# Kernel optimization log

Hardware: AMD Instinct MI355X
Metric: run time of the kernel (lower is better)

## Reference

```python
import jax, jax.numpy as jnp
import numpy as np

D_MODEL = 1024
N_LAYERS = 4
EXPAND = 2
D_CONV = 4
D_STATE = 16
INTER = EXPAND * D_MODEL          # 2048
DT_RANK = (D_MODEL + 15) // 16    # 64, HF: math.ceil(d_model/16)
B_SZ = 4
SEQ = 1024
EPS = 1e-5


def setup_inputs() -> dict:
    key = jax.random.key(0)
    ks = jax.random.split(key, 8)
    nrm = lambda k, s: (0.02 * jax.random.normal(k, s)).astype(jnp.float32)
    return {
        "x": jax.random.normal(ks[0], (B_SZ, SEQ, D_MODEL), dtype=jnp.float32),
        "in_w": nrm(ks[1], (N_LAYERS, 2 * INTER, D_MODEL)),           # in_proj (no bias)
        "conv_w": nrm(ks[2], (N_LAYERS, INTER, D_CONV)),              # depthwise conv weight
        "conv_b": jnp.zeros((N_LAYERS, INTER), jnp.float32),           # conv bias
        "x_w": nrm(ks[3], (N_LAYERS, DT_RANK + 2 * D_STATE, INTER)),  # x_proj (no bias)
        "dt_w": nrm(ks[4], (N_LAYERS, INTER, DT_RANK)),               # dt_proj weight
        "dt_b": jax.random.uniform(ks[5], (N_LAYERS, INTER), minval=-4.0, maxval=-2.0).astype(jnp.float32),
        "A_log": jnp.tile(jnp.log(jnp.arange(1, D_STATE + 1, dtype=jnp.float32)), (N_LAYERS, INTER, 1)),
        "D": jnp.ones((N_LAYERS, INTER), jnp.float32),
        "out_w": nrm(ks[6], (N_LAYERS, D_MODEL, INTER)),              # out_proj (no bias)
        "norm_w": jnp.ones((N_LAYERS, D_MODEL), jnp.float32),          # per-block RMSNorm
        "norm_f_w": jnp.ones((D_MODEL,), jnp.float32),                 # final RMSNorm
    }


def _rmsnorm(x, w):
    return x * jax.lax.rsqrt(jnp.mean(x * x, axis=-1, keepdims=True) + EPS) * w


def _mixer(x, in_w, conv_w, conv_b, x_w, dt_w, dt_b, A_log, Dp, out_w):
    # x: [B, L, d_model]
    Bb = x.shape[0]
    proj = x @ in_w.T                              # [B, L, 2I]
    hs, gate = jnp.split(proj, 2, axis=-1)          # each [B, L, I]
    # causal depthwise conv over time
    hc = hs.transpose(0, 2, 1)                      # [B, I, L]
    hc = jnp.pad(hc, ((0, 0), (0, 0), (D_CONV - 1, 0)))
    hc = jax.lax.conv_general_dilated(
        hc, conv_w[:, None, :], (1,), 'VALID',
        dimension_numbers=('NCH', 'OIH', 'NCH'), feature_group_count=INTER)
    hc = hc + conv_b[None, :, None]
    u = jax.nn.silu(hc).transpose(0, 2, 1)          # [B, L, I]
    ssm = u @ x_w.T                                 # [B, L, dt_rank + 2N]
    dt, Bm, Cm = jnp.split(ssm, [DT_RANK, DT_RANK + D_STATE], axis=-1)
    dt = jax.nn.softplus(dt @ dt_w.T + dt_b)        # [B, L, I]
    A = -jnp.exp(A_log)                             # [I, N]

    def step(state, xs):
        dt_t, B_t, C_t, u_t = xs                    # [B,I], [B,N], [B,N], [B,I]
        dA = jnp.exp(dt_t[:, :, None] * A[None])    # [B, I, N]
        state = dA * state + (dt_t * u_t)[:, :, None] * B_t[:, None, :]
        y = jnp.einsum('bin,bn->bi', state, C_t)
        return state, y

    init = jnp.zeros((Bb, INTER, D_STATE), x.dtype)
    xs = (dt.transpose(1, 0, 2), Bm.transpose(1, 0, 2),
          Cm.transpose(1, 0, 2), u.transpose(1, 0, 2))
    _, ys = jax.lax.scan(step, init, xs)            # ys: [L, B, I]
    y = ys.transpose(1, 0, 2) + u * Dp              # skip term D * u
    y = y * jax.nn.silu(gate)
    return y @ out_w.T                              # [B, L, d_model]


def reference(x, in_w, conv_w, conv_b, x_w, dt_w, dt_b, A_log, D, out_w, norm_w, norm_f_w):
    h = x
    for l in range(N_LAYERS):
        h = h + _mixer(_rmsnorm(h, norm_w[l]), in_w[l], conv_w[l], conv_b[l],
                       x_w[l], dt_w[l], dt_b[l], A_log[l], D[l], out_w[l])
    return _rmsnorm(h, norm_f_w)
```

## Files before the change

kernel.cpp:

```cpp
#include <hip/hip_runtime.h>
#include <hip/hip_bf16.h>
#include <math.h>

#define D_MODEL 1024
#define N_LAYERS 4
#define INTER 2048
#define D_CONV 4
#define D_STATE 16
#define DT_RANK 64
#define B_SZ 4
#define SEQ 1024
#define TOK (B_SZ*SEQ)
#define XROWS 128
#define EPSV 1e-5f
#define GCH 64
#define TC (SEQ/GCH)
#define KSPL 8
#define OSPL 2

typedef unsigned short u16;
typedef unsigned int u32;
typedef __attribute__((ext_vector_type(8))) short bf16x8;
typedef __attribute__((ext_vector_type(4))) short s16x4;
typedef __attribute__((ext_vector_type(4))) float f32x4;

__device__ __forceinline__ u16 f2b(float f) {
    union { float f; unsigned u; } v; v.f = f;
    unsigned r = v.u + 0x7fffu + ((v.u >> 16) & 1u);
    return (u16)(r >> 16);
}
__device__ __forceinline__ float b2f(u16 h) {
    union { unsigned u; float f; } v; v.u = ((unsigned)h) << 16;
    return v.f;
}
__device__ __forceinline__ float silu(float x) {
    return x / (1.f + __expf(-x));
}
__device__ __forceinline__ void gload16(const void* g, void* l) {
    __builtin_amdgcn_global_load_lds(
        (const __attribute__((address_space(1))) void*)g,
        (__attribute__((address_space(3))) void*)l, 16, 0, 0);
}

__global__ __launch_bounds__(512, 2)
void gemm256_k(const u16* __restrict__ A, const u16* __restrict__ B,
               u16* __restrict__ C, int K, int ldc)
{
    __shared__ u16 lds[2][2][256 * 64];
    const int tid  = threadIdx.x;
    const int lane = tid & 63;
    const int wid  = tid >> 6;
    const int wr   = wid >> 2;
    const int wc   = wid & 3;
    const int hwid = blockIdx.y * gridDim.x + blockIdx.x;
    const int work = (hwid & 7) * 32 + (hwid >> 3);
    const int row0 = (work >> 4) * 256;
    const int col0 = (work & 15) * 256;
    const int r16   = lane & 15;
    const int khalf = lane >> 4;

    auto ld1 = [&](int buf, int k0, int l) {
        int op = l >> 2;
        int c  = tid + (l & 3) * 512;
        int r  = c >> 3;
        int ds = c & 7;
        int sc = (ds ^ (r & 7)) * 8;
        const u16* src = op ? &B[(size_t)(col0 + r) * K + k0 + sc]
                            : &A[(size_t)(row0 + r) * K + k0 + sc];
        gload16(src, &lds[buf][op][c * 8]);
    };
    auto stage2 = [&](int buf, int k0, int pair) {
        if (pair == 0)      { ld1(buf, k0, 0); ld1(buf, k0, 2); }
        else if (pair == 1) { ld1(buf, k0, 4); ld1(buf, k0, 5); }
        else if (pair == 2) { ld1(buf, k0, 6); ld1(buf, k0, 7); }
        else                { ld1(buf, k0, 1); ld1(buf, k0, 3); }
    };
    auto rdA = [&](int buf, int mrow, int ks) -> bf16x8 {
        int row  = wr * 128 + mrow + r16;
        int phys = ((ks << 2) | khalf) ^ (row & 7);
        return *(const bf16x8*)&lds[buf][0][row * 64 + phys * 8];
    };
    auto rdB = [&](int buf, int nrow, int ks) -> bf16x8 {
        int row  = wc * 64 + nrow + r16;
        int phys = ((ks << 2) | khalf) ^ (row & 7);
        return *(const bf16x8*)&lds[buf][1][row * 64 + phys * 8];
    };

    f32x4 acc[8][4];
#pragma unroll
    for (int m = 0; m < 8; ++m)
#pragma unroll
        for (int n = 0; n < 4; ++n)
            acc[m][n] = (f32x4)0.f;

    bf16x8 af[4][2], bf2[2][2];

#define PHASE_MFMA(MH, NH) do {                                               \
    asm volatile("s_waitcnt lgkmcnt(0)" ::: "memory");                        \
    __builtin_amdgcn_sched_barrier(0);                                        \
    __builtin_amdgcn_s_setprio(1);                                            \
    _Pragma("unroll")                                                         \
    for (int ks = 0; ks < 2; ++ks)                                            \
        _Pragma("unroll")                                                     \
        for (int m = 0; m < 4; ++m)                                           \
            _Pragma("unroll")                                                 \
            for (int n = 0; n < 2; ++n)                                       \
                acc[(MH)*4+m][(NH)*2+n] =                                     \
                    __builtin_amdgcn_mfma_f32_16x16x32_bf16(                  \
                        af[m][ks], bf2[n][ks], acc[(MH)*4+m][(NH)*2+n],0,0,0);\
    __builtin_amdgcn_s_setprio(0);                                            \
} while (0)

    const int nt = K >> 6;
    stage2(0, 0, 0); stage2(0, 0, 1); stage2(0, 0, 2); stage2(0, 0, 3);
    asm volatile("s_waitcnt vmcnt(2)" ::: "memory");
    __builtin_amdgcn_s_barrier();

    for (int j = 0; j < nt; ++j) {
        const int buf = j & 1;
        const int nb  = buf ^ 1;
        const int k1  = (j + 1) << 6;
        const bool pf = (j + 1 < nt);
        if (pf) stage2(nb, k1, 0);
#pragma unroll
        for (int m = 0; m < 4; ++m) {
            af[m][0] = rdA(buf, m * 16, 0); af[m][1] = rdA(buf, m * 16, 1);
        }
#pragma unroll
        for (int n = 0; n < 2; ++n) {
            bf2[n][0] = rdB(buf, n * 16, 0); bf2[n][1] = rdB(buf, n * 16, 1);
        }
        __builtin_amdgcn_s_barrier();
        PHASE_MFMA(0, 0);
        __builtin_amdgcn_s_barrier();
        if (pf) stage2(nb, k1, 1);
#pragma unroll
        for (int n = 0; n < 2; ++n) {
            bf2[n][0] = rdB(buf, 32 + n * 16, 0); bf2[n][1] = rdB(buf, 32 + n * 16, 1);
        }
        __builtin_amdgcn_s_barrier();
        PHASE_MFMA(0, 1);
        if (pf) { asm volatile("s_waitcnt vmcnt(4)" ::: "memory"); }
        else    { asm volatile("s_waitcnt vmcnt(0)" ::: "memory"); }
        __builtin_amdgcn_s_barrier();
        if (pf) stage2(nb, k1, 2);
#pragma unroll
        for (int m = 0; m < 4; ++m) {
            af[m][0] = rdA(buf, 64 + m * 16, 0); af[m][1] = rdA(buf, 64 + m * 16, 1);
        }
        __builtin_amdgcn_s_barrier();
        PHASE_MFMA(1, 1);
        __builtin_amdgcn_s_barrier();
        if (pf) stage2(nb, k1, 3);
#pragma unroll
        for (int n = 0; n < 2; ++n) {
            bf2[n][0] = rdB(buf, n * 16, 0); bf2[n][1] = rdB(buf, n * 16, 1);
        }
        __builtin_amdgcn_s_barrier();
        PHASE_MFMA(1, 0);
        asm volatile("s_waitcnt vmcnt(2)" ::: "memory");
        __builtin_amdgcn_s_barrier();
    }
#undef PHASE_MFMA

    const int orow = row0 + wr * 128;
    const int ocol = col0 + wc * 64;
#pragma unroll
    for (int am = 0; am < 8; ++am)
#pragma unroll
        for (int an = 0; an < 4; ++an)
#pragma unroll
            for (int r = 0; r < 4; ++r) {
                int rr = orow + am * 16 + khalf * 4 + r;
                int cc = ocol + an * 16 + r16;
                C[(size_t)rr * ldc + cc] = f2b(acc[am][an][r]);
            }
}

template<int EPI, int NPX = 1>
__global__ __launch_bounds__(256)
void gemm_bt(const u16* __restrict__ A, const u16* __restrict__ B,
             void* __restrict__ C, const float* __restrict__ aux,
             int K, int lda, int ldc, size_t pstride)
{
    __shared__ u16 As[3][128 * 32];
    __shared__ u16 Bs[3][128 * 32];
    const int tid  = threadIdx.x;
    const int lane = tid & 63;
    const int w    = tid >> 6;
    const int wr   = w >> 1, wc = w & 1;
    const int row0 = blockIdx.y * 128;
    int col0 = blockIdx.x * 128;
    if (EPI == 4) {
        int part = blockIdx.x / NPX;
        col0 = (blockIdx.x % NPX) * 128;
        A += (size_t)part * K;
        B += (size_t)part * K;
        C = (void*)((float*)C + (size_t)part * pstride);
    }
    const int r16   = lane & 15;
    const int khalf = lane >> 4;
    const int kslot = khalf ^ ((r16 >> 1) & 3);

    auto stage = [&](int buf, int k0) {
#pragma unroll
        for (int c = 0; c < 2; ++c) {
            int chunk = tid + c * 256;
            int r  = chunk >> 2;
            int j  = chunk & 3;
            int k8 = (j ^ ((r >> 1) & 3)) * 8;
            gload16(&A[(size_t)(row0 + r) * lda + k0 + k8], &As[buf][chunk * 8]);
            gload16(&B[(size_t)(col0 + r) * lda + k0 + k8], &Bs[buf][chunk * 8]);
        }
    };

    f32x4 acc[4][4];
#pragma unroll
    for (int m = 0; m < 4; ++m)
#pragma unroll
        for (int n = 0; n < 4; ++n)
            acc[m][n] = (f32x4)0.f;

    const int nt = K >> 5;
    stage(0, 0);
    if (nt > 1) stage(1, 32);

    int cur = 0, sb = 2;
    for (int t = 0; t < nt; ++t) {
        if (t + 2 < nt) {
            stage(sb, (t + 2) << 5);
            asm volatile("s_waitcnt vmcnt(8)" ::: "memory");
        } else if (t + 1 < nt) {
            asm volatile("s_waitcnt vmcnt(4)" ::: "memory");
        } else {
            asm volatile("s_waitcnt vmcnt(0)" ::: "memory");
        }
        __builtin_amdgcn_s_barrier();

        bf16x8 af[4], bfr[4];
#pragma unroll
        for (int m = 0; m < 4; ++m)
            af[m]  = *(const bf16x8*)&As[cur][(wr * 64 + m * 16 + r16) * 32 + kslot * 8];
#pragma unroll
        for (int n = 0; n < 4; ++n)
            bfr[n] = *(const bf16x8*)&Bs[cur][(wc * 64 + n * 16 + r16) * 32 + kslot * 8];
#pragma unroll
        for (int m = 0; m < 4; ++m)
#pragma unroll
            for (int n = 0; n < 4; ++n)
                acc[m][n] = __builtin_amdgcn_mfma_f32_16x16x32_bf16(
                    af[m], bfr[n], acc[m][n], 0, 0, 0);

        __builtin_amdgcn_sched_barrier(0);
        asm volatile("s_waitcnt lgkmcnt(0)" ::: "memory");
        __builtin_amdgcn_s_barrier();
        cur = (cur == 2) ? 0 : cur + 1;
        sb  = (sb  == 2) ? 0 : sb  + 1;
    }

    const int orow = row0 + wr * 64;
    const int ocol = col0 + wc * 64;
#pragma unroll
    for (int m = 0; m < 4; ++m)
#pragma unroll
        for (int n = 0; n < 4; ++n) {
#pragma unroll
            for (int r = 0; r < 4; ++r) {
                int rr = orow + m * 16 + khalf * 4 + r;
                int cc = ocol + n * 16 + r16;
                float v = acc[m][n][r];
                size_t o = (size_t)rr * ldc + cc;
                if (EPI == 0 || EPI == 4) {
                    ((float*)C)[o] = v;
                } else if (EPI == 2) {
                    float x = v + aux[cc];
                    float sp = (x > 20.f) ? x : log1pf(__expf(x));
                    ((u16*)C)[o] = f2b(sp);
                }
            }
        }
}

__global__ __launch_bounds__(256)
void xred_k(const float* __restrict__ part, float* __restrict__ ssm,
            u16* __restrict__ dtr)
{
    int idx = blockIdx.x * 256 + threadIdx.x;
    int row = idx >> 5;
    int col = (idx & 31) * 4;
    size_t o = (size_t)row * XROWS + col;
    const size_t stride = (size_t)TOK * XROWS;
    f32x4 v = *(const f32x4*)&part[o];
#pragma unroll
    for (int p = 1; p < KSPL; ++p)
        v += *(const f32x4*)&part[o + p * stride];
    *(f32x4*)&ssm[o] = v;
    if (col < DT_RANK) {
        s16x4 d;
#pragma unroll
        for (int j = 0; j < 4; ++j) d[j] = (short)f2b(v[j]);
        *(s16x4*)&dtr[(size_t)row * DT_RANK + col] = d;
    }
}

template<int OUTBF>
__global__ __launch_bounds__(256)
void rmsnorm_k(const float* __restrict__ in, const float* __restrict__ w,
               void* __restrict__ out)
{
    __shared__ float red[4];
    const int row = blockIdx.x;
    const int tid = threadIdx.x;
    const float* r = in + (size_t)row * D_MODEL;
    f32x4 v = *(const f32x4*)&r[tid * 4];
    float ss = v[0]*v[0] + v[1]*v[1] + v[2]*v[2] + v[3]*v[3];
#pragma unroll
    for (int m = 32; m >= 1; m >>= 1) ss += __shfl_xor(ss, m, 64);
    if ((tid & 63) == 0) red[tid >> 6] = ss;
    __syncthreads();
    if (tid == 0) {
        float s = red[0] + red[1] + red[2] + red[3];
        red[0] = rsqrtf(s / (float)D_MODEL + EPSV);
    }
    __syncthreads();
    float sc = red[0];
    if (OUTBF) {
        u16* o = (u16*)out + (size_t)row * D_MODEL + tid * 4;
#pragma unroll
        for (int j = 0; j < 4; ++j) o[j] = f2b(v[j] * sc * w[tid * 4 + j]);
    } else {
        float* o = (float*)out + (size_t)row * D_MODEL + tid * 4;
#pragma unroll
        for (int j = 0; j < 4; ++j) o[j] = v[j] * sc * w[tid * 4 + j];
    }
}

template<int OUTBF, int WRITEH>
__global__ __launch_bounds__(256)
void rmsnorm_res_k(const float* __restrict__ hin, const float* __restrict__ p,
                   const float* __restrict__ w, float* __restrict__ hout,
                   void* __restrict__ out)
{
    __shared__ float red[4];
    const int row = blockIdx.x;
    const int tid = threadIdx.x;
    const size_t o4 = (size_t)row * D_MODEL + tid * 4;
    f32x4 v  = *(const f32x4*)&hin[o4];
    f32x4 p0 = *(const f32x4*)&p[o4];
    f32x4 p1 = *(const f32x4*)&p[(size_t)TOK * D_MODEL + o4];
    v += p0 + p1;
    if (WRITEH) *(f32x4*)&hout[o4] = v;
    float ss = v[0]*v[0] + v[1]*v[1] + v[2]*v[2] + v[3]*v[3];
#pragma unroll
    for (int m = 32; m >= 1; m >>= 1) ss += __shfl_xor(ss, m, 64);
    if ((tid & 63) == 0) red[tid >> 6] = ss;
    __syncthreads();
    if (tid == 0) {
        float s = red[0] + red[1] + red[2] + red[3];
        red[0] = rsqrtf(s / (float)D_MODEL + EPSV);
    }
    __syncthreads();
    float sc = red[0];
    if (OUTBF) {
        u16* o = (u16*)out + o4;
#pragma unroll
        for (int j = 0; j < 4; ++j) o[j] = f2b(v[j] * sc * w[tid * 4 + j]);
    } else {
        float* o = (float*)out + o4;
#pragma unroll
        for (int j = 0; j < 4; ++j) o[j] = v[j] * sc * w[tid * 4 + j];
    }
}

__global__ __launch_bounds__(256)
void conv_silu_k(const u16* __restrict__ projbf, const float* __restrict__ w,
                 const float* __restrict__ bias, u16* __restrict__ ubf)
{
    const int row = blockIdx.x;
    const int t   = row & (SEQ - 1);
    const int i0  = threadIdx.x * 8;
    float acc[8];
    {
        f32x4 b0 = *(const f32x4*)&bias[i0];
        f32x4 b1 = *(const f32x4*)&bias[i0 + 4];
#pragma unroll
        for (int j = 0; j < 4; ++j) { acc[j] = b0[j]; acc[j + 4] = b1[j]; }
    }
    f32x4 wv[8];
#pragma unroll
    for (int j = 0; j < 8; ++j)
        wv[j] = *(const f32x4*)&w[(i0 + j) * 4];
#pragma unroll
    for (int k = 0; k < 4; ++k) {
        int tt = t - 3 + k;
        if (tt >= 0) {
            bf16x8 hv = *(const bf16x8*)&projbf[(size_t)(row - 3 + k) * 4096 + i0];
#pragma unroll
            for (int j = 0; j < 8; ++j)
                acc[j] += b2f((u16)hv[j]) * wv[j][k];
        }
    }
    bf16x8 o;
#pragma unroll
    for (int j = 0; j < 8; ++j)
        o[j] = (short)f2b(silu(acc[j]));
    *(bf16x8*)&ubf[(size_t)row * INTER + i0] = o;
}

__global__ __launch_bounds__(256)
void achk_k(const float* __restrict__ Alog, int* __restrict__ flags)
{
    int idx = blockIdx.x * 256 + threadIdx.x;
    if (idx >= N_LAYERS * INTER * D_STATE) return;
    int l = idx / (INTER * D_STATE);
    int n = idx & (D_STATE - 1);
    float ref = logf((float)(n + 1));
    if (fabsf(Alog[idx] - ref) > 1e-4f) atomicAnd(&flags[l], 0);
}

#define POWCH(W, p) \
    float p##2=(W)*(W), p##3=p##2*(W), p##4=p##2*p##2, p##5=p##4*(W),        \
          p##6=p##4*p##2, p##7=p##4*p##3, p##8=p##4*p##4, p##9=p##8*(W),     \
          p##10=p##8*p##2, p##11=p##8*p##3, p##12=p##8*p##4, p##13=p##8*p##5,\
          p##14=p##8*p##6, p##15=p##8*p##7, p##16=p##8*p##8;

#define SUPD(S, B, du, w1) \
    S[0]=w1*S[0]+du*B[0][0];   S[1]=w1##2*S[1]+du*B[0][1];                   \
    S[2]=w1##3*S[2]+du*B[0][2];  S[3]=w1##4*S[3]+du*B[0][3];                 \
    S[4]=w1##5*S[4]+du*B[1][0];  S[5]=w1##6*S[5]+du*B[1][1];                 \
    S[6]=w1##7*S[6]+du*B[1][2];  S[7]=w1##8*S[7]+du*B[1][3];                 \
    S[8]=w1##9*S[8]+du*B[2][0];  S[9]=w1##10*S[9]+du*B[2][1];                \
    S[10]=w1##11*S[10]+du*B[2][2]; S[11]=w1##12*S[11]+du*B[2][3];            \
    S[12]=w1##13*S[12]+du*B[3][0]; S[13]=w1##14*S[13]+du*B[3][1];            \
    S[14]=w1##15*S[14]+du*B[3][2]; S[15]=w1##16*S[15]+du*B[3][3];

#define YDOT(S, Cv) \
    (S[0]*Cv[0][0]+S[1]*Cv[0][1]+S[2]*Cv[0][2]+S[3]*Cv[0][3]                 \
    +S[4]*Cv[1][0]+S[5]*Cv[1][1]+S[6]*Cv[1][2]+S[7]*Cv[1][3]                 \
    +S[8]*Cv[2][0]+S[9]*Cv[2][1]+S[10]*Cv[2][2]+S[11]*Cv[2][3]               \
    +S[12]*Cv[3][0]+S[13]*Cv[3][1]+S[14]*Cv[3][2]+S[15]*Cv[3][3])

__global__ __launch_bounds__(256)
void scan1_k(const u16* __restrict__ dtbf, const u16* __restrict__ ubf,
             const float* __restrict__ ssm, const float* __restrict__ Alog,
             const int* __restrict__ flag,
             float* __restrict__ cst, float* __restrict__ dts)
{
    __shared__ float Bsh[TC][D_STATE];
    const int tid = threadIdx.x;
    const int i2  = blockIdx.x * 256 + tid;
    const int c0  = i2 * 2;
    const int g   = blockIdx.y;
    const int b   = blockIdx.z;
    const int t0  = g * TC;
    {
        int t = tid >> 4, n = tid & 15;
        Bsh[t][n] = ssm[(size_t)(b * SEQ + t0 + t) * XROWS + DT_RANK + n];
    }
    __syncthreads();

    float s0[D_STATE], s1[D_STATE];
#pragma unroll
    for (int n = 0; n < D_STATE; ++n) { s0[n] = 0.f; s1[n] = 0.f; }
    float ds0 = 0.f, ds1 = 0.f;

    const u32* dtp = (const u32*)dtbf + ((size_t)(b * SEQ + t0) * INTER >> 1) + i2;
    const u32* up  = (const u32*)ubf  + ((size_t)(b * SEQ + t0) * INTER >> 1) + i2;

    if (flag[0]) {
#pragma unroll
        for (int t = 0; t < TC; ++t) {
            u32 dp = dtp[(size_t)t * (INTER / 2)];
            u32 uq = up[(size_t)t * (INTER / 2)];
            float dta = b2f((u16)dp), dtb = b2f((u16)(dp >> 16));
            float ua  = b2f((u16)uq), ub  = b2f((u16)(uq >> 16));
            float dua = dta * ua, dub = dtb * ub;
            ds0 += dta; ds1 += dtb;
            float wa = __expf(-dta), wb = __expf(-dtb);
            POWCH(wa, wa) POWCH(wb, wb)
            f32x4 Bq[4];
#pragma unroll
            for (int q = 0; q < 4; ++q) Bq[q] = *(const f32x4*)&Bsh[t][q * 4];
            SUPD(s0, Bq, dua, wa)
            SUPD(s1, Bq, dub, wb)
        }
    } else {
        float a0[D_STATE], a1[D_STATE];
#pragma unroll
        for (int n = 0; n < D_STATE; ++n) {
            a0[n] = -__expf(Alog[(size_t)c0 * D_STATE + n]);
            a1[n] = -__expf(Alog[(size_t)(c0 + 1) * D_STATE + n]);
        }
        for (int t = 0; t < TC; ++t) {
            u32 dp = dtp[(size_t)t * (INTER / 2)];
            u32 uq = up[(size_t)t * (INTER / 2)];
            float dta = b2f((u16)dp), dtb = b2f((u16)(dp >> 16));
            float ua  = b2f((u16)uq), ub  = b2f((u16)(uq >> 16));
            float dua = dta * ua, dub = dtb * ub;
            ds0 += dta; ds1 += dtb;
#pragma unroll
            for (int n = 0; n < D_STATE; ++n) {
                float Bn = Bsh[t][n];
                s0[n] = __expf(dta * a0[n]) * s0[n] + dua * Bn;
                s1[n] = __expf(dtb * a1[n]) * s1[n] + dub * Bn;
            }
        }
    }
    size_t o = ((size_t)(b * GCH + g) * INTER + c0) * D_STATE;
#pragma unroll
    for (int n = 0; n < D_STATE; n += 4) {
        f32x4 v0 = { s0[n], s0[n+1], s0[n+2], s0[n+3] };
        f32x4 v1 = { s1[n], s1[n+1], s1[n+2], s1[n+3] };
        *(f32x4*)&cst[o + n] = v0;
        *(f32x4*)&cst[o + D_STATE + n] = v1;
    }
    size_t od = (size_t)(b * GCH + g) * INTER + c0;
    dts[od] = ds0; dts[od + 1] = ds1;
}

__global__ __launch_bounds__(256)
void scan2_k(float* __restrict__ cst, const float* __restrict__ dts,
             const float* __restrict__ Alog)
{
    int idx = blockIdx.x * 256 + threadIdx.x;
    int sub = idx & 3;
    int i   = (idx >> 2) & (INTER - 1);
    int b   = idx >> 13;
    int n0  = sub * 4;
    float a[4];
#pragma unroll
    for (int n = 0; n < 4; ++n)
        a[n] = -__expf(Alog[(size_t)i * D_STATE + n0 + n]);
    f32x4 s = (f32x4)0.f;
    for (int g = 0; g < GCH; ++g) {
        size_t o = ((size_t)(b * GCH + g) * INTER + i) * D_STATE + n0;
        f32x4 tmp = *(const f32x4*)&cst[o];
        *(f32x4*)&cst[o] = s;
        float d = dts[(size_t)(b * GCH + g) * INTER + i];
#pragma unroll
        for (int n = 0; n < 4; ++n)
            s[n] = __expf(a[n] * d) * s[n] + tmp[n];
    }
}

__global__ __launch_bounds__(256)
void scan3_k(const u16* __restrict__ dtbf, const u16* __restrict__ ubf,
             const float* __restrict__ ssm, const u16* __restrict__ projbf,
             const float* __restrict__ Alog, const float* __restrict__ Dp,
             const int* __restrict__ flag,
             const float* __restrict__ sst, u16* __restrict__ ybf)
{
    __shared__ float Bsh[TC][D_STATE];
    __shared__ float Csh[TC][D_STATE];
    const int tid = threadIdx.x;
    const int i2  = blockIdx.x * 256 + tid;
    const int c0  = i2 * 2;
    const int g   = blockIdx.y;
    const int b   = blockIdx.z;
    const int t0  = g * TC;
    {
        int t = tid >> 4, n = tid & 15;
        size_t row = (size_t)(b * SEQ + t0 + t) * XROWS;
        Bsh[t][n] = ssm[row + DT_RANK + n];
        Csh[t][n] = ssm[row + DT_RANK + D_STATE + n];
    }
    __syncthreads();

    const float Da = Dp[c0], Db = Dp[c0 + 1];
    float s0[D_STATE], s1[D_STATE];
    size_t so = ((size_t)(b * GCH + g) * INTER + c0) * D_STATE;
#pragma unroll
    for (int n = 0; n < D_STATE; n += 4) {
        f32x4 v0 = *(const f32x4*)&sst[so + n];
        f32x4 v1 = *(const f32x4*)&sst[so + D_STATE + n];
        s0[n] = v0[0]; s0[n+1] = v0[1]; s0[n+2] = v0[2]; s0[n+3] = v0[3];
        s1[n] = v1[0]; s1[n+1] = v1[1]; s1[n+2] = v1[2]; s1[n+3] = v1[3];
    }

    const u32* dtp = (const u32*)dtbf + ((size_t)(b * SEQ + t0) * INTER >> 1) + i2;
    const u32* up  = (const u32*)ubf  + ((size_t)(b * SEQ + t0) * INTER >> 1) + i2;
    const u32* gp  = (const u32*)projbf + (((size_t)(b * SEQ + t0) * 4096 + INTER) >> 1) + i2;
    u32*       yp  = (u32*)ybf + ((size_t)(b * SEQ + t0) * INTER >> 1) + i2;

    if (flag[0]) {
#pragma unroll
        for (int t = 0; t < TC; ++t) {
            u32 dp = dtp[(size_t)t * (INTER / 2)];
            u32 uq = up[(size_t)t * (INTER / 2)];
            u32 gq = gp[(size_t)t * (4096 / 2)];
            float dta = b2f((u16)dp), dtb = b2f((u16)(dp >> 16));
            float ua  = b2f((u16)uq), ub  = b2f((u16)(uq >> 16));
            float ga  = b2f((u16)gq), gb  = b2f((u16)(gq >> 16));
            float dua = dta * ua, dub = dtb * ub;
            float wa = __expf(-dta), wb = __expf(-dtb);
            POWCH(wa, wa) POWCH(wb, wb)
            f32x4 Bq[4], Cq[4];
#pragma unroll
            for (int q = 0; q < 4; ++q) {
                Bq[q] = *(const f32x4*)&Bsh[t][q * 4];
                Cq[q] = *(const f32x4*)&Csh[t][q * 4];
            }
            SUPD(s0, Bq, dua, wa)
            SUPD(s1, Bq, dub, wb)
            float y0 = YDOT(s0, Cq);
            float y1 = YDOT(s1, Cq);
            y0 = (y0 + Da * ua) * silu(ga);
            y1 = (y1 + Db * ub) * silu(gb);
            yp[(size_t)t * (INTER / 2)] = (u32)f2b(y0) | ((u32)f2b(y1) << 16);
        }
    } else {
        float a0[D_STATE], a1[D_STATE];
#pragma unroll
        for (int n = 0; n < D_STATE; ++n) {
            a0[n] = -__expf(Alog[(size_t)c0 * D_STATE + n]);
            a1[n] = -__expf(Alog[(size_t)(c0 + 1) * D_STATE + n]);
        }
        for (int t = 0; t < TC; ++t) {
            u32 dp = dtp[(size_t)t * (INTER / 2)];
            u32 uq = up[(size_t)t * (INTER / 2)];
            u32 gq = gp[(size_t)t * (4096 / 2)];
            float dta = b2f((u16)dp), dtb = b2f((u16)(dp >> 16));
            float ua  = b2f((u16)uq), ub  = b2f((u16)(uq >> 16));
            float ga  = b2f((u16)gq), gb  = b2f((u16)(gq >> 16));
            float dua = dta * ua, dub = dtb * ub;
            float y0 = 0.f, y1 = 0.f;
#pragma unroll
            for (int n = 0; n < D_STATE; ++n) {
                float Bn = Bsh[t][n], Cn = Csh[t][n];
                s0[n] = __expf(dta * a0[n]) * s0[n] + dua * Bn;
                s1[n] = __expf(dtb * a1[n]) * s1[n] + dub * Bn;
                y0 += s0[n] * Cn; y1 += s1[n] * Cn;
            }
            y0 = (y0 + Da * ua) * silu(ga);
            y1 = (y1 + Db * ub) * silu(gb);
            yp[(size_t)t * (INTER / 2)] = (u32)f2b(y0) | ((u32)f2b(y1) << 16);
        }
    }
}

__global__ __launch_bounds__(256)
void cvt_f2b_k(const float* __restrict__ in, u16* __restrict__ out, int n)
{
    int idx = (blockIdx.x * 256 + threadIdx.x) * 4;
    if (idx >= n) return;
    f32x4 v = *(const f32x4*)&in[idx];
    s16x4 d;
#pragma unroll
    for (int j = 0; j < 4; ++j) d[j] = (short)f2b(v[j]);
    *(s16x4*)&out[idx] = d;
}

__global__ __launch_bounds__(256)
void pad_xw_k(const float* __restrict__ xw, u16* __restrict__ out)
{
    int idx = (blockIdx.x * 256 + threadIdx.x) * 4;
    if (idx >= N_LAYERS * XROWS * INTER) return;
    int l = idx / (XROWS * INTER);
    int r = (idx >> 11) & (XROWS - 1);
    int c = idx & (INTER - 1);
    s16x4 d;
    if (r < 96) {
        f32x4 v = *(const f32x4*)&xw[((size_t)l * 96 + r) * INTER + c];
#pragma unroll
        for (int j = 0; j < 4; ++j) d[j] = (short)f2b(v[j]);
    } else {
        d = (s16x4)0;
    }
    *(s16x4*)&out[idx] = d;
}

extern "C" void kernel_launch(void* const* d_in, const int* in_sizes, int n_in,
                              void* d_out, int out_size, void* d_ws, size_t ws_size,
                              hipStream_t stream)
{
    const float* x      = (const float*)d_in[0];
    const float* in_w   = (const float*)d_in[1];
    const float* conv_w = (const float*)d_in[2];
    const float* conv_b = (const float*)d_in[3];
    const float* x_w    = (const float*)d_in[4];
    const float* dt_w   = (const float*)d_in[5];
    const float* dt_b   = (const float*)d_in[6];
    const float* A_log  = (const float*)d_in[7];
    const float* Dp     = (const float*)d_in[8];
    const float* out_w  = (const float*)d_in[9];
    const float* norm_w = (const float*)d_in[10];
    const float* norm_f = (const float*)d_in[11];

    char* ws = (char*)d_ws;
    size_t off = 0;
    auto alloc = [&](size_t bytes) { char* p = ws + off; off += (bytes + 255) & ~(size_t)255; return p; };

    u16*   inw_bf  = (u16*)  alloc((size_t)N_LAYERS * 4096 * 1024 * 2);
    u16*   xw_bf   = (u16*)  alloc((size_t)N_LAYERS * XROWS * INTER * 2);
    u16*   dtw_bf  = (u16*)  alloc((size_t)N_LAYERS * INTER * DT_RANK * 2);
    u16*   outw_bf = (u16*)  alloc((size_t)N_LAYERS * D_MODEL * INTER * 2);
    float* h       = (float*)alloc((size_t)TOK * D_MODEL * 4);
    u16*   xn_bf   = (u16*)  alloc((size_t)TOK * D_MODEL * 2);
    u16*   proj_bf = (u16*)  alloc((size_t)TOK * 4096 * 2);
    u16*   u_bf    = (u16*)  alloc((size_t)TOK * INTER * 2);
    float* ssm     = (float*)alloc((size_t)TOK * XROWS * 4);
    float* parts   = (float*)alloc((size_t)OSPL * TOK * D_MODEL * 4);
    u16*   dtr_bf  = (u16*)  alloc((size_t)TOK * DT_RANK * 2);
    u16*   dt_bf   = (u16*)  alloc((size_t)TOK * INTER * 2);
    u16*   y_bf    = (u16*)  alloc((size_t)TOK * INTER * 2);
    float* cst     = (float*)alloc((size_t)B_SZ * GCH * INTER * D_STATE * 4);
    float* dts     = (float*)alloc((size_t)B_SZ * GCH * INTER * 4);
    int*   aflags  = (int*)  alloc(N_LAYERS * sizeof(int));
    (void)ws_size; (void)n_in; (void)in_sizes; (void)out_size;

    {
        int n = N_LAYERS * 4096 * 1024;
        cvt_f2b_k<<<n / 1024, 256, 0, stream>>>(in_w, inw_bf, n);
        int np = N_LAYERS * XROWS * INTER;
        pad_xw_k<<<np / 1024, 256, 0, stream>>>(x_w, xw_bf);
        int nd = N_LAYERS * INTER * DT_RANK;
        cvt_f2b_k<<<nd / 1024, 256, 0, stream>>>(dt_w, dtw_bf, nd);
        int no = N_LAYERS * D_MODEL * INTER;
        cvt_f2b_k<<<no / 1024, 256, 0, stream>>>(out_w, outw_bf, no);
        hipMemsetAsync(aflags, 0xFF, N_LAYERS * sizeof(int), stream);
        int na = N_LAYERS * INTER * D_STATE;
        achk_k<<<(na + 255) / 256, 256, 0, stream>>>(A_log, aflags);
    }

    for (int l = 0; l < N_LAYERS; ++l) {
        if (l == 0)
            rmsnorm_k<1><<<TOK, 256, 0, stream>>>(x, norm_w, xn_bf);
        else
            rmsnorm_res_k<1, 1><<<TOK, 256, 0, stream>>>(
                (l == 1) ? x : h, parts, norm_w + (size_t)l * D_MODEL, h, xn_bf);
        gemm256_k<<<dim3(16, 16), 512, 0, stream>>>(
            xn_bf, inw_bf + (size_t)l * 4096 * 1024, proj_bf, 1024, 4096);
        conv_silu_k<<<TOK, 256, 0, stream>>>(
            proj_bf, conv_w + (size_t)l * INTER * D_CONV, conv_b + (size_t)l * INTER, u_bf);
        gemm_bt<4, 1><<<dim3(KSPL, 32), 256, 0, stream>>>(
            u_bf, xw_bf + (size_t)l * XROWS * INTER, parts, nullptr,
            INTER / KSPL, INTER, XROWS, (size_t)TOK * XROWS);
        xred_k<<<(TOK * 32) / 256, 256, 0, stream>>>(parts, ssm, dtr_bf);
        gemm_bt<2><<<dim3(16, 32), 256, 0, stream>>>(
            dtr_bf, dtw_bf + (size_t)l * INTER * DT_RANK, dt_bf,
            dt_b + (size_t)l * INTER, DT_RANK, DT_RANK, INTER, 0);
        scan1_k<<<dim3(INTER / 512, GCH, B_SZ), 256, 0, stream>>>(
            dt_bf, u_bf, ssm, A_log + (size_t)l * INTER * D_STATE, aflags + l, cst, dts);
        scan2_k<<<(B_SZ * INTER * 4) / 256, 256, 0, stream>>>(
            cst, dts, A_log + (size_t)l * INTER * D_STATE);
        scan3_k<<<dim3(INTER / 512, GCH, B_SZ), 256, 0, stream>>>(
            dt_bf, u_bf, ssm, proj_bf, A_log + (size_t)l * INTER * D_STATE,
            Dp + (size_t)l * INTER, aflags + l, cst, y_bf);
        gemm_bt<4, 8><<<dim3(OSPL * 8, 32), 256, 0, stream>>>(
            y_bf, outw_bf + (size_t)l * D_MODEL * INTER, parts, nullptr,
            INTER / OSPL, INTER, D_MODEL, (size_t)TOK * D_MODEL);
    }
    rmsnorm_res_k<0, 0><<<TOK, 256, 0, stream>>>(
        h, parts, norm_f, nullptr, d_out);
}
```

Before: 900.7 us.

## Reorder GEMM MFMA phases, batch conv tokens, and merge weight conversion kernels

The 256-tile GEMM main loop now uses separate A and B fragment registers and visits quadrants in a snake order (00,10,11,01), so each phase reloads only half the fragments. The LDS stage and vmcnt waits are reordered to match. The causal conv+SiLU kernel now handles 4 tokens per block and reuses 7 loaded rows instead of reloading 4 rows per token. The four weight conversion and padding kernels are merged into one launch. Together these cut LDS reads, redundant global loads and launch count, at the cost of more registers and more delicate wait-count correctness.

Result: faster. 856.9 us, median of 2 (-4.9%).

```diff
diff --git a/kernel.cpp b/kernel.cpp
--- a/kernel.cpp
+++ b/kernel.cpp
@@ -93,9 +93,9 @@
         for (int n = 0; n < 4; ++n)
             acc[m][n] = (f32x4)0.f;
 
-    bf16x8 af[4][2], bf2[2][2];
-
-#define PHASE_MFMA(MH, NH) do {                                               \
+    bf16x8 afA[4][2], afB[4][2], b01[2][2], b23[2][2];
+
+#define PHASE_MFMA(MH, NH, AF, BF) do {                                       \
     asm volatile("s_waitcnt lgkmcnt(0)" ::: "memory");                        \
     __builtin_amdgcn_sched_barrier(0);                                        \
     __builtin_amdgcn_s_setprio(1);                                            \
@@ -107,13 +107,13 @@
             for (int n = 0; n < 2; ++n)                                       \
                 acc[(MH)*4+m][(NH)*2+n] =                                     \
                     __builtin_amdgcn_mfma_f32_16x16x32_bf16(                  \
-                        af[m][ks], bf2[n][ks], acc[(MH)*4+m][(NH)*2+n],0,0,0);\
+                        AF[m][ks], BF[n][ks], acc[(MH)*4+m][(NH)*2+n],0,0,0); \
     __builtin_amdgcn_s_setprio(0);                                            \
 } while (0)
 
     const int nt = K >> 6;
-    stage2(0, 0, 0); stage2(0, 0, 1); stage2(0, 0, 2); stage2(0, 0, 3);
-    asm volatile("s_waitcnt vmcnt(2)" ::: "memory");
+    stage2(0, 0, 0); stage2(0, 0, 1); stage2(0, 0, 3); stage2(0, 0, 2);
+    asm volatile("s_waitcnt vmcnt(4)" ::: "memory");
     __builtin_amdgcn_s_barrier();
 
     for (int j = 0; j < nt; ++j) {
@@ -124,41 +124,38 @@
         if (pf) stage2(nb, k1, 0);
 #pragma unroll
         for (int m = 0; m < 4; ++m) {
-            af[m][0] = rdA(buf, m * 16, 0); af[m][1] = rdA(buf, m * 16, 1);
+            afA[m][0] = rdA(buf, m * 16, 0); afA[m][1] = rdA(buf, m * 16, 1);
         }
 #pragma unroll
         for (int n = 0; n < 2; ++n) {
-            bf2[n][0] = rdB(buf, n * 16, 0); bf2[n][1] = rdB(buf, n * 16, 1);
-        }
-        __builtin_amdgcn_s_barrier();
-        PHASE_MFMA(0, 0);
+            b01[n][0] = rdB(buf, n * 16, 0); b01[n][1] = rdB(buf, n * 16, 1);
+        }
+        __builtin_amdgcn_s_barrier();
+        PHASE_MFMA(0, 0, afA, b01);
+        if (pf) { asm volatile("s_waitcnt vmcnt(4)" ::: "memory"); }
+        else    { asm volatile("s_waitcnt vmcnt(2)" ::: "memory"); }
         __builtin_amdgcn_s_barrier();
         if (pf) stage2(nb, k1, 1);
 #pragma unroll
-        for (int n = 0; n < 2; ++n) {
-            bf2[n][0] = rdB(buf, 32 + n * 16, 0); bf2[n][1] = rdB(buf, 32 + n * 16, 1);
-        }
-        __builtin_amdgcn_s_barrier();
-        PHASE_MFMA(0, 1);
+        for (int m = 0; m < 4; ++m) {
+            afB[m][0] = rdA(buf, 64 + m * 16, 0); afB[m][1] = rdA(buf, 64 + m * 16, 1);
+        }
+        __builtin_amdgcn_s_barrier();
+        PHASE_MFMA(1, 0, afB, b01);
         if (pf) { asm volatile("s_waitcnt vmcnt(4)" ::: "memory"); }
         else    { asm volatile("s_waitcnt vmcnt(0)" ::: "memory"); }
         __builtin_amdgcn_s_barrier();
+        if (pf) stage2(nb, k1, 3);
+#pragma unroll
+        for (int n = 0; n < 2; ++n) {
+            b23[n][0] = rdB(buf, 32 + n * 16, 0); b23[n][1] = rdB(buf, 32 + n * 16, 1);
+        }
+        __builtin_amdgcn_s_barrier();
+        PHASE_MFMA(1, 1, afB, b23);
+        __builtin_amdgcn_s_barrier();
         if (pf) stage2(nb, k1, 2);
-#pragma unroll
-        for (int m = 0; m < 4; ++m) {
-            af[m][0] = rdA(buf, 64 + m * 16, 0); af[m][1] = rdA(buf, 64 + m * 16, 1);
-        }
-        __builtin_amdgcn_s_barrier();
-        PHASE_MFMA(1, 1);
-        __builtin_amdgcn_s_barrier();
-        if (pf) stage2(nb, k1, 3);
-#pragma unroll
-        for (int n = 0; n < 2; ++n) {
-            bf2[n][0] = rdB(buf, n * 16, 0); bf2[n][1] = rdB(buf, n * 16, 1);
-        }
-        __builtin_amdgcn_s_barrier();
-        PHASE_MFMA(1, 0);
-        asm volatile("s_waitcnt vmcnt(2)" ::: "memory");
+        PHASE_MFMA(0, 1, afA, b23);
+        if (pf) { asm volatile("s_waitcnt vmcnt(4)" ::: "memory"); }
         __builtin_amdgcn_s_barrier();
     }
 #undef PHASE_MFMA
@@ -376,35 +373,46 @@
 void conv_silu_k(const u16* __restrict__ projbf, const float* __restrict__ w,
                  const float* __restrict__ bias, u16* __restrict__ ubf)
 {
-    const int row = blockIdx.x;
-    const int t   = row & (SEQ - 1);
-    const int i0  = threadIdx.x * 8;
-    float acc[8];
+    const int tok0 = blockIdx.x * 4;
+    const int t0   = tok0 & (SEQ - 1);
+    const int i0   = threadIdx.x * 8;
+    float hv[7][8];
+#pragma unroll
+    for (int m = 0; m < 7; ++m) {
+        int tt = t0 - 3 + m;
+        if (tt >= 0) {
+            bf16x8 v = *(const bf16x8*)&projbf[(size_t)(tok0 - 3 + m) * 4096 + i0];
+#pragma unroll
+            for (int j = 0; j < 8; ++j) hv[m][j] = b2f((u16)v[j]);
+        } else {
+#pragma unroll
+            for (int j = 0; j < 8; ++j) hv[m][j] = 0.f;
+        }
+    }
+    f32x4 wv[8];
+#pragma unroll
+    for (int j = 0; j < 8; ++j)
+        wv[j] = *(const f32x4*)&w[(i0 + j) * 4];
+    float bs[8];
     {
         f32x4 b0 = *(const f32x4*)&bias[i0];
         f32x4 b1 = *(const f32x4*)&bias[i0 + 4];
 #pragma unroll
-        for (int j = 0; j < 4; ++j) { acc[j] = b0[j]; acc[j + 4] = b1[j]; }
-    }
-    f32x4 wv[8];
-#pragma unroll
-    for (int j = 0; j < 8; ++j)
-        wv[j] = *(const f32x4*)&w[(i0 + j) * 4];
-#pragma unroll
-    for (int k = 0; k < 4; ++k) {
-        int tt = t - 3 + k;
-        if (tt >= 0) {
-            bf16x8 hv = *(const bf16x8*)&projbf[(size_t)(row - 3 + k) * 4096 + i0];
-#pragma unroll
-            for (int j = 0; j < 8; ++j)
-                acc[j] += b2f((u16)hv[j]) * wv[j][k];
-        }
-    }
-    bf16x8 o;
-#pragma unroll
-    for (int j = 0; j < 8; ++j)
-        o[j] = (short)f2b(silu(acc[j]));
-    *(bf16x8*)&ubf[(size_t)row * INTER + i0] = o;
+        for (int j = 0; j < 4; ++j) { bs[j] = b0[j]; bs[j + 4] = b1[j]; }
+    }
+#pragma unroll
+    for (int q = 0; q < 4; ++q) {
+        bf16x8 o;
+#pragma unroll
+        for (int j = 0; j < 8; ++j) {
+            float acc = bs[j];
+#pragma unroll
+            for (int k = 0; k < 4; ++k)
+                acc += hv[q + k][j] * wv[j][k];
+            o[j] = (short)f2b(silu(acc));
+        }
+        *(bf16x8*)&ubf[(size_t)(tok0 + q) * INTER + i0] = o;
+    }
 }
 
 __global__ __launch_bounds__(256)
@@ -638,35 +646,48 @@
     }
 }
 
-__global__ __launch_bounds__(256)
-void cvt_f2b_k(const float* __restrict__ in, u16* __restrict__ out, int n)
+#define INW_N  (N_LAYERS * 4096 * 1024)
+#define DTW_N  (N_LAYERS * INTER * DT_RANK)
+#define OUTW_N (N_LAYERS * D_MODEL * INTER)
+#define XWP_N  (N_LAYERS * XROWS * INTER)
+__global__ __launch_bounds__(256)
+void cvtall_k(const float* __restrict__ in_w, const float* __restrict__ dt_w,
+              const float* __restrict__ out_w, const float* __restrict__ xw,
+              u16* __restrict__ inw_bf, u16* __restrict__ dtw_bf,
+              u16* __restrict__ outw_bf, u16* __restrict__ xw_bf)
 {
     int idx = (blockIdx.x * 256 + threadIdx.x) * 4;
-    if (idx >= n) return;
-    f32x4 v = *(const f32x4*)&in[idx];
+    const float* src;
+    u16* dst;
+    int i;
+    if (idx < INW_N) {
+        src = in_w; dst = inw_bf; i = idx;
+    } else if (idx < INW_N + DTW_N) {
+        src = dt_w; dst = dtw_bf; i = idx - INW_N;
+    } else if (idx < INW_N + DTW_N + OUTW_N) {
+        src = out_w; dst = outw_bf; i = idx - INW_N - DTW_N;
+    } else {
+        i = idx - INW_N - DTW_N - OUTW_N;
+        if (i >= XWP_N) return;
+        int l = i / (XROWS * INTER);
+        int r = (i >> 11) & (XROWS - 1);
+        int c = i & (INTER - 1);
+        s16x4 d;
+        if (r < 96) {
+            f32x4 v = *(const f32x4*)&xw[((size_t)l * 96 + r) * INTER + c];
+#pragma unroll
+            for (int j = 0; j < 4; ++j) d[j] = (short)f2b(v[j]);
+        } else {
+            d = (s16x4)0;
+        }
+        *(s16x4*)&xw_bf[i] = d;
+        return;
+    }
+    f32x4 v = *(const f32x4*)&src[i];
     s16x4 d;
 #pragma unroll
     for (int j = 0; j < 4; ++j) d[j] = (short)f2b(v[j]);
-    *(s16x4*)&out[idx] = d;
-}
-
-__global__ __launch_bounds__(256)
-void pad_xw_k(const float* __restrict__ xw, u16* __restrict__ out)
-{
-    int idx = (blockIdx.x * 256 + threadIdx.x) * 4;
-    if (idx >= N_LAYERS * XROWS * INTER) return;
-    int l = idx / (XROWS * INTER);
-    int r = (idx >> 11) & (XROWS - 1);
-    int c = idx & (INTER - 1);
-    s16x4 d;
-    if (r < 96) {
-        f32x4 v = *(const f32x4*)&xw[((size_t)l * 96 + r) * INTER + c];
-#pragma unroll
-        for (int j = 0; j < 4; ++j) d[j] = (short)f2b(v[j]);
-    } else {
-        d = (s16x4)0;
-    }
-    *(s16x4*)&out[idx] = d;
+    *(s16x4*)&dst[i] = d;
 }
 
 extern "C" void kernel_launch(void* const* d_in, const int* in_sizes, int n_in,
@@ -709,14 +730,9 @@
     (void)ws_size; (void)n_in; (void)in_sizes; (void)out_size;
 
     {
-        int n = N_LAYERS * 4096 * 1024;
-        cvt_f2b_k<<<n / 1024, 256, 0, stream>>>(in_w, inw_bf, n);
-        int np = N_LAYERS * XROWS * INTER;
-        pad_xw_k<<<np / 1024, 256, 0, stream>>>(x_w, xw_bf);
-        int nd = N_LAYERS * INTER * DT_RANK;
-        cvt_f2b_k<<<nd / 1024, 256, 0, stream>>>(dt_w, dtw_bf, nd);
-        int no = N_LAYERS * D_MODEL * INTER;
-        cvt_f2b_k<<<no / 1024, 256, 0, stream>>>(out_w, outw_bf, no);
+        int total = INW_N + DTW_N + OUTW_N + XWP_N;
+        cvtall_k<<<(total / 4 + 255) / 256, 256, 0, stream>>>(
+            in_w, dt_w, out_w, x_w, inw_bf, dtw_bf, outw_bf, xw_bf);
         hipMemsetAsync(aflags, 0xFF, N_LAYERS * sizeof(int), stream);
         int na = N_LAYERS * INTER * D_STATE;
         achk_k<<<(na + 255) / 256, 256, 0, stream>>>(A_log, aflags);
@@ -730,7 +746,7 @@
                 (l == 1) ? x : h, parts, norm_w + (size_t)l * D_MODEL, h, xn_bf);
         gemm256_k<<<dim3(16, 16), 512, 0, stream>>>(
             xn_bf, inw_bf + (size_t)l * 4096 * 1024, proj_bf, 1024, 4096);
-        conv_silu_k<<<TOK, 256, 0, stream>>>(
+        conv_silu_k<<<TOK / 4, 256, 0, stream>>>(
             proj_bf, conv_w + (size_t)l * INTER * D_CONV, conv_b + (size_t)l * INTER, u_bf);
         gemm_bt<4, 1><<<dim3(KSPL, 32), 256, 0, stream>>>(
             u_bf, xw_bf + (size_t)l * XROWS * INTER, parts, nullptr,
```
